# Kernel tuning notes

Measured on AMD Instinct MI355X. Metric: run time of the kernel, lower is better.

## Reference

```python
import jax, jax.numpy as jnp
import numpy as np

B, S, D, H = 4, 2048, 1024, 16
DEPTH = D // H
NEG = -1e9


def setup_inputs() -> dict:
    key = jax.random.key(0)
    ks = jax.random.split(key, 9)
    scale = 1.0 / np.sqrt(D)
    x = jax.random.normal(ks[0], (B, S, D), dtype=jnp.float32)
    # causal additive mask: 1 where future positions (masked), 0 elsewhere
    mask = jnp.triu(jnp.ones((S, S), dtype=jnp.float32), k=1)[None, None, :, :]
    wq = jax.random.normal(ks[1], (D, D), dtype=jnp.float32) * scale
    bq = jnp.zeros((D,), dtype=jnp.float32)
    wk = jax.random.normal(ks[2], (D, D), dtype=jnp.float32) * scale
    bk = jnp.zeros((D,), dtype=jnp.float32)
    wv = jax.random.normal(ks[3], (D, D), dtype=jnp.float32) * scale
    bv = jnp.zeros((D,), dtype=jnp.float32)
    wo = jax.random.normal(ks[4], (D, D), dtype=jnp.float32) * scale
    bo = jnp.zeros((D,), dtype=jnp.float32)
    return {"x": x, "mask": mask, "wq": wq, "bq": bq, "wk": wk, "bk": bk,
            "wv": wv, "bv": bv, "wo": wo, "bo": bo}


def _split_heads(t):
    # [B, S, D] -> [B, H, S, depth]
    return t.reshape(B, S, H, DEPTH).transpose(0, 2, 1, 3)


def reference(x, mask, wq, bq, wk, bk, wv, bv, wo, bo):
    q = _split_heads(x @ wq.T + bq)
    k = _split_heads(x @ wk.T + bk)
    v = _split_heads(x @ wv.T + bv)
    scores = jnp.einsum('bhqd,bhkd->bhqk', q, k) / jnp.sqrt(jnp.float32(DEPTH))
    scores = scores + mask * NEG
    attn = jax.nn.softmax(scores, axis=-1)
    out = jnp.einsum('bhqk,bhkd->bhqd', attn, v)  # [B, H, S, depth]
    out = out.transpose(0, 2, 1, 3).reshape(B, S, D)
    return out @ wo.T + bo
```

## Files before the change

### kernel.cpp

```cpp
#include <hip/hip_runtime.h>
#include <hip/hip_bf16.h>
#include <stdint.h>

typedef __attribute__((ext_vector_type(8))) short short8;
typedef __attribute__((ext_vector_type(4))) float f32x4;
typedef __attribute__((ext_vector_type(16))) float f32x16;

#define AS1 __attribute__((address_space(1)))
#define AS3 __attribute__((address_space(3)))

constexpr int Bc = 4, Sc = 2048, Dc = 1024, Hc = 16;

__device__ __forceinline__ unsigned short f2b(float x) {
  __hip_bfloat16 h = __float2bfloat16(x);
  return *reinterpret_cast<unsigned short*>(&h);
}

__device__ __forceinline__ uint32_t cvtpk(float lo, float hi) {
  uint32_t r;
  asm("v_cvt_pk_bf16_f32 %0, %1, %2" : "=v"(r) : "v"(lo), "v"(hi));
  return r;
}

__device__ __forceinline__ void glds16(const void* g, void* l) {
  __builtin_amdgcn_global_load_lds((const AS1 uint32_t*)g, (AS3 uint32_t*)l, 16, 0, 0);
}

__global__ void cast_f32_bf16_x4(const float* __restrict__ in,
                                 unsigned short* __restrict__ out, int n4) {
  int i = blockIdx.x * blockDim.x + threadIdx.x;
  if (i >= n4) return;
  float4 a = ((const float4*)in)[i];
  ushort4 o;
  o.x = f2b(a.x); o.y = f2b(a.y); o.z = f2b(a.z); o.w = f2b(a.w);
  ((ushort4*)out)[i] = o;
}

__global__ void cast_w4(const float* __restrict__ wq, const float* __restrict__ wk,
                        const float* __restrict__ wv, const float* __restrict__ wo,
                        unsigned short* __restrict__ oq, unsigned short* __restrict__ ok,
                        unsigned short* __restrict__ ov, unsigned short* __restrict__ oo) {
  int which = blockIdx.y;
  const float* in = which == 0 ? wq : which == 1 ? wk : which == 2 ? wv : wo;
  unsigned short* out = which == 0 ? oq : which == 1 ? ok : which == 2 ? ov : oo;
  int i = blockIdx.x * blockDim.x + threadIdx.x;
  float4 a = ((const float4*)in)[i];
  ushort4 o;
  o.x = f2b(a.x); o.y = f2b(a.y); o.z = f2b(a.z); o.w = f2b(a.w);
  ((ushort4*)out)[i] = o;
}

template<int MODE>
__device__ __forceinline__ void gemm128_b32(
    const unsigned short* __restrict__ A, const unsigned short* __restrict__ W,
    const float* __restrict__ bias, void* __restrict__ outp,
    int m0, int n0, unsigned short* lA, unsigned short* lB)
{
  const int tid = threadIdx.x;
  const int w = tid >> 6, lane = tid & 63;
  const int g = lane >> 4, c = lane & 15;
  const int wr = w >> 1, wc = w & 1;

  f32x4 acc[4][4];
#pragma unroll
  for (int i = 0; i < 4; ++i)
#pragma unroll
    for (int j = 0; j < 4; ++j) acc[i][j] = f32x4{0.f, 0.f, 0.f, 0.f};

  const int srow = lane >> 2;
  const int schunk = (lane & 3) * 8;

  for (int k0 = 0; k0 < 1024; k0 += 32) {
#pragma unroll
    for (int i = 0; i < 2; ++i) {
      int row = i * 64 + w * 16 + srow;
      glds16(A + (size_t)(m0 + row) * 1024 + k0 + schunk,
             (char*)lA + i * 4096 + w * 1024);
      glds16(W + (size_t)(n0 + row) * 1024 + k0 + schunk,
             (char*)lB + i * 4096 + w * 1024);
    }
    __syncthreads();

    short8 aF[4], bF[4];
#pragma unroll
    for (int mt = 0; mt < 4; ++mt) {
      int row = wr * 64 + mt * 16 + c;
      aF[mt] = *(const short8*)&lA[row * 32 + g * 8];
    }
#pragma unroll
    for (int nt = 0; nt < 4; ++nt) {
      int row = wc * 64 + nt * 16 + c;
      bF[nt] = *(const short8*)&lB[row * 32 + g * 8];
    }
#pragma unroll
    for (int mt = 0; mt < 4; ++mt)
#pragma unroll
      for (int nt = 0; nt < 4; ++nt)
        acc[mt][nt] = __builtin_amdgcn_mfma_f32_16x16x32_bf16(aF[mt], bF[nt],
                                                              acc[mt][nt], 0, 0, 0);
    __syncthreads();
  }

#pragma unroll
  for (int mt = 0; mt < 4; ++mt) {
    int mg = m0 + wr * 64 + mt * 16 + 4 * g;
#pragma unroll
    for (int nt = 0; nt < 4; ++nt) {
      int ng = n0 + wc * 64 + nt * 16 + c;
      float bb_ = bias[ng];
      if constexpr (MODE == 0) {
        unsigned short* o = (unsigned short*)outp;
#pragma unroll
        for (int r = 0; r < 4; ++r)
          o[(size_t)(mg + r) * 1024 + ng] = f2b(acc[mt][nt][r] + bb_);
      } else if constexpr (MODE == 1) {
        unsigned short* o = (unsigned short*)outp;
        int bb = mg >> 11, s0 = mg & 2047;
        int hh = ng >> 6, dd = ng & 63;
        ushort4 pk;
        pk.x = f2b(acc[mt][nt][0] + bb_);
        pk.y = f2b(acc[mt][nt][1] + bb_);
        pk.z = f2b(acc[mt][nt][2] + bb_);
        pk.w = f2b(acc[mt][nt][3] + bb_);
        *(ushort4*)&o[(((size_t)bb * Hc + hh) * 64 + dd) * Sc + s0] = pk;
      } else {
        float* o = (float*)outp;
#pragma unroll
        for (int r = 0; r < 4; ++r)
          o[(size_t)(mg + r) * 1024 + ng] = acc[mt][nt][r] + bb_;
      }
    }
  }
}

template<int MODE>
__device__ __forceinline__ void gemm128_b64(
    const unsigned short* __restrict__ A, const unsigned short* __restrict__ W,
    const float* __restrict__ bias, void* __restrict__ outp,
    int m0, int n0, unsigned short* lA, unsigned short* lB)
{
  const int tid = threadIdx.x;
  const int w = tid >> 6, lane = tid & 63;
  const int g = lane >> 4, c = lane & 15;
  const int wr = w >> 1, wc = w & 1;

  f32x4 acc[4][4];
#pragma unroll
  for (int i = 0; i < 4; ++i)
#pragma unroll
    for (int j = 0; j < 4; ++j) acc[i][j] = f32x4{0.f, 0.f, 0.f, 0.f};

  const int lrow8 = lane >> 3;
  const int gslot = (lane & 7) ^ lrow8;

  const unsigned short* ap[4];
  const unsigned short* bp[4];
#pragma unroll
  for (int j = 0; j < 4; ++j) {
    int row = (j * 4 + w) * 8 + lrow8;
    ap[j] = A + (size_t)(m0 + row) * 1024 + gslot * 8;
    bp[j] = W + (size_t)(n0 + row) * 1024 + gslot * 8;
  }

  const int sl0 = (g ^ (c & 7)) << 4;
  const int sl1 = ((4 ^ g) ^ (c & 7)) << 4;
  const char* lA0 = (const char*)lA + (wr * 64 + c) * 128 + sl0;
  const char* lA1 = (const char*)lA + (wr * 64 + c) * 128 + sl1;
  const char* lB0 = (const char*)lB + (wc * 64 + c) * 128 + sl0;
  const char* lB1 = (const char*)lB + (wc * 64 + c) * 128 + sl1;

#define STAGE64                                             \
  do {                                                      \
    _Pragma("unroll")                                       \
    for (int j = 0; j < 4; ++j) {                           \
      glds16(ap[j], (char*)lA + (j * 4 + w) * 1024);        \
      glds16(bp[j], (char*)lB + (j * 4 + w) * 1024);        \
      ap[j] += 64; bp[j] += 64;                             \
    }                                                       \
  } while (0)

  STAGE64;
  for (int t = 0; t < 16; ++t) {
    asm volatile("s_waitcnt vmcnt(0)" ::: "memory");
    __builtin_amdgcn_s_barrier();
    asm volatile("" ::: "memory");

#pragma unroll
    for (int ks = 0; ks < 2; ++ks) {
      short8 aF[4], bF[4];
#pragma unroll
      for (int mt = 0; mt < 4; ++mt)
        aF[mt] = *(const short8*)((ks ? lA1 : lA0) + mt * 2048);
#pragma unroll
      for (int nt = 0; nt < 4; ++nt)
        bF[nt] = *(const short8*)((ks ? lB1 : lB0) + nt * 2048);
#pragma unroll
      for (int mt = 0; mt < 4; ++mt)
#pragma unroll
        for (int nt = 0; nt < 4; ++nt)
          acc[mt][nt] = __builtin_amdgcn_mfma_f32_16x16x32_bf16(
              aF[mt], bF[nt], acc[mt][nt], 0, 0, 0);
    }
    asm volatile("" ::: "memory");
    __builtin_amdgcn_s_barrier();
    asm volatile("" ::: "memory");
    if (t + 1 < 16) STAGE64;
  }
#undef STAGE64

#pragma unroll
  for (int mt = 0; mt < 4; ++mt) {
    int mg = m0 + wr * 64 + mt * 16 + 4 * g;
#pragma unroll
    for (int nt = 0; nt < 4; ++nt) {
      int ng = n0 + wc * 64 + nt * 16 + c;
      float bb_ = bias[ng];
      if constexpr (MODE == 2) {
        float* o = (float*)outp;
#pragma unroll
        for (int r = 0; r < 4; ++r)
          o[(size_t)(mg + r) * 1024 + ng] = acc[mt][nt][r] + bb_;
      } else {
        unsigned short* o = (unsigned short*)outp;
#pragma unroll
        for (int r = 0; r < 4; ++r)
          o[(size_t)(mg + r) * 1024 + ng] = f2b(acc[mt][nt][r] + bb_);
      }
    }
  }
}

__global__ __launch_bounds__(256) void qkv_gemm(
    const unsigned short* __restrict__ xb,
    const unsigned short* __restrict__ wqb, const unsigned short* __restrict__ wkb,
    const unsigned short* __restrict__ wvb,
    const float* __restrict__ bq, const float* __restrict__ bk,
    const float* __restrict__ bv,
    unsigned short* __restrict__ qo, unsigned short* __restrict__ ko,
    unsigned short* __restrict__ vto)
{
  __shared__ unsigned short lA[128 * 32], lB[128 * 32];
  int m0 = blockIdx.x * 128;
  int which = blockIdx.y >> 3;
  int n0 = (blockIdx.y & 7) * 128;
  if (which == 0)      gemm128_b32<0>(xb, wqb, bq, qo, m0, n0, lA, lB);
  else if (which == 1) gemm128_b32<0>(xb, wkb, bk, ko, m0, n0, lA, lB);
  else                 gemm128_b32<1>(xb, wvb, bv, vto, m0, n0, lA, lB);
}

__global__ __launch_bounds__(256) void out_gemm(
    const unsigned short* __restrict__ ao, const unsigned short* __restrict__ wob,
    const float* __restrict__ bo, float* __restrict__ out)
{
  __shared__ unsigned short lA[128 * 64], lB[128 * 64];
  gemm128_b64<2>(ao, wob, bo, out, blockIdx.x * 128, blockIdx.y * 128, lA, lB);
}

__global__ __launch_bounds__(256, 2) void attn_kernel(
    const unsigned short* __restrict__ qg, const unsigned short* __restrict__ kg,
    const unsigned short* __restrict__ vtg, unsigned short* __restrict__ ao)
{
  __shared__ unsigned short lK[2][64 * 64];
  __shared__ unsigned short lV[2][64 * 64];

  const int bh = blockIdx.x;
  const int qlo = blockIdx.y, qhi = 15 - qlo;
  const int b = bh >> 4, h = bh & 15;
  const int tid = threadIdx.x, w = tid >> 6, lane = tid & 63;
  const int qr = lane & 31, hi = lane >> 5;
  const int qb2[2] = { qlo * 128 + 32 * w, qhi * 128 + 32 * w };
  constexpr float CE = 0.125f * 1.44269504f;

  short8 qB[2][4];
#pragma unroll
  for (int qi = 0; qi < 2; ++qi) {
    const unsigned short* qp = qg + (size_t)(b * Sc + qb2[qi] + qr) * Dc + h * 64 + 8 * hi;
#pragma unroll
    for (int i = 0; i < 4; ++i)
      qB[qi][i] = *(const short8*)(qp + 16 * i);
  }

  float m_[2] = { -3e38f, -3e38f }, lv[2] = { 0.f, 0.f };
  f32x16 oT[2][2];
#pragma unroll
  for (int qi = 0; qi < 2; ++qi)
#pragma unroll
    for (int n = 0; n < 2; ++n)
#pragma unroll
      for (int r = 0; r < 16; ++r) oT[qi][n][r] = 0.f;

  const int srow8 = lane >> 3;
  const int sslot = lane & 7;
  const unsigned short* kb_ = kg + (size_t)b * Sc * Dc + h * 64;
  const unsigned short* vb_ = vtg + (size_t)bh * 64 * Sc;

  auto stage = [&](int buf, int t) {
    const int kv0 = t * 64;
#pragma unroll
    for (int i = 0; i < 2; ++i) {
      int row = i * 32 + w * 8 + srow8;
      int gch = sslot ^ (row & 7);
      glds16(kb_ + (size_t)(kv0 + row) * Dc + gch * 8,
             (char*)lK[buf] + i * 4096 + w * 1024);
      glds16(vb_ + (size_t)row * Sc + kv0 + gch * 8,
             (char*)lV[buf] + i * 4096 + w * 1024);
    }
  };

  const int ntl = 2 * (qhi + 1);
  stage(0, 0);
  asm volatile("s_waitcnt vmcnt(0)" ::: "memory");
  __builtin_amdgcn_s_barrier();
  asm volatile("" ::: "memory");

  for (int t = 0; t < ntl; ++t) {
    const int cur = t & 1;
    const int kv0 = t * 64;
    if (t + 1 < ntl) stage(cur ^ 1, t + 1);

    if (kv0 <= qb2[1] + 31) {
      short8 kA[2][4];
#pragma unroll
      for (int kblk = 0; kblk < 2; ++kblk) {
        const int row = kblk * 32 + qr;
        const int swz = (row & 7) << 4;
#pragma unroll
        for (int i = 0; i < 4; ++i)
          kA[kblk][i] = *(const short8*)((const char*)lK[cur] + row * 128 +
                          (((2 * i + hi) * 16) ^ swz));
      }

      short8 pB[2][4];
      bool act[2];
#pragma unroll
      for (int qi = 0; qi < 2; ++qi) {
        const int qbase = qb2[qi];
        act[qi] = (kv0 <= qbase + 31);
        if (!act[qi]) continue;

        f32x16 sT[2];
        __builtin_amdgcn_s_setprio(1);
#pragma unroll
        for (int kblk = 0; kblk < 2; ++kblk) {
          f32x16 s;
#pragma unroll
          for (int r = 0; r < 16; ++r) s[r] = 0.f;
#pragma unroll
          for (int i = 0; i < 4; ++i)
            s = __builtin_amdgcn_mfma_f32_32x32x16_bf16(kA[kblk][i], qB[qi][i],
                                                        s, 0, 0, 0);
          sT[kblk] = s;
        }
        __builtin_amdgcn_s_setprio(0);

        if (kv0 + 63 > qbase) {
          const int q = qbase + qr;
#pragma unroll
          for (int kblk = 0; kblk < 2; ++kblk)
#pragma unroll
            for (int r = 0; r < 16; ++r) {
              int k = kv0 + kblk * 32 + (r & 3) + 8 * (r >> 2) + 4 * hi;
              if (k > q) sT[kblk][r] = -1e30f;
            }
        }

        float mx = sT[0][0];
#pragma unroll
        for (int r = 1; r < 16; ++r) mx = fmaxf(mx, sT[0][r]);
#pragma unroll
        for (int r = 0; r < 16; ++r) mx = fmaxf(mx, sT[1][r]);
        mx = fmaxf(mx, __shfl_xor(mx, 32));

        if (!__all(mx <= m_[qi] + 64.f)) {
          const float mo = m_[qi];
          const float mn = fmaxf(mo, mx);
          const float sf = __builtin_amdgcn_exp2f((mo - mn) * CE);
          m_[qi] = mn;
          lv[qi] *= sf;
#pragma unroll
          for (int n = 0; n < 2; ++n)
#pragma unroll
            for (int r = 0; r < 16; ++r) oT[qi][n][r] *= sf;
        }
        const float mc = m_[qi] * CE;
        float ls = 0.f;
#pragma unroll
        for (int kblk = 0; kblk < 2; ++kblk)
#pragma unroll
          for (int r = 0; r < 16; ++r) {
            float p = __builtin_amdgcn_exp2f(sT[kblk][r] * CE - mc);
            sT[kblk][r] = p;
            ls += p;
          }
        lv[qi] += ls;

#pragma unroll
        for (int kblk = 0; kblk < 2; ++kblk) {
          uint32_t pk[4][2];
#pragma unroll
          for (int qp = 0; qp < 4; ++qp)
#pragma unroll
            for (int rp = 0; rp < 2; ++rp)
              pk[qp][rp] = cvtpk(sT[kblk][4 * qp + 2 * rp],
                                 sT[kblk][4 * qp + 2 * rp + 1]);
#pragma unroll
          for (int m2 = 0; m2 < 2; ++m2) {
            uint32_t s0 = hi ? pk[2 * m2][0] : pk[2 * m2 + 1][0];
            uint32_t s1 = hi ? pk[2 * m2][1] : pk[2 * m2 + 1][1];
            uint32_t r0 = __shfl_xor(s0, 32);
            uint32_t r1 = __shfl_xor(s1, 32);
            uint32_t w0 = hi ? r0 : pk[2 * m2][0];
            uint32_t w1 = hi ? r1 : pk[2 * m2][1];
            uint32_t w2 = hi ? pk[2 * m2 + 1][0] : r0;
            uint32_t w3 = hi ? pk[2 * m2 + 1][1] : r1;
            uint32_t tmp[4] = { w0, w1, w2, w3 };
            pB[qi][2 * kblk + m2] = *(const short8*)tmp;
          }
        }
      }

      short8 vA[2][4];
#pragma unroll
      for (int n = 0; n < 2; ++n) {
        const int row = 32 * n + qr;
        const int swz = (row & 7) << 4;
#pragma unroll
        for (int m = 0; m < 4; ++m)
          vA[n][m] = *(const short8*)((const char*)lV[cur] + row * 128 +
                       (((2 * m + hi) * 16) ^ swz));
      }

      __builtin_amdgcn_s_setprio(1);
#pragma unroll
      for (int qi = 0; qi < 2; ++qi) {
        if (!act[qi]) continue;
#pragma unroll
        for (int n = 0; n < 2; ++n)
#pragma unroll
          for (int m = 0; m < 4; ++m)
            oT[qi][n] = __builtin_amdgcn_mfma_f32_32x32x16_bf16(
                vA[n][m], pB[qi][m], oT[qi][n], 0, 0, 0);
      }
      __builtin_amdgcn_s_setprio(0);
    }

    asm volatile("s_waitcnt vmcnt(0)" ::: "memory");
    __builtin_amdgcn_s_barrier();
    asm volatile("" ::: "memory");
  }

#pragma unroll
  for (int qi = 0; qi < 2; ++qi) {
    float l = lv[qi] + __shfl_xor(lv[qi], 32);
    float inv = 1.0f / l;
    const int qrow = qb2[qi] + qr;
    unsigned short* op = ao + (size_t)(b * Sc + qrow) * Dc + h * 64;
#pragma unroll
    for (int n = 0; n < 2; ++n)
#pragma unroll
      for (int rg = 0; rg < 4; ++rg) {
        ushort4 pkv;
        pkv.x = f2b(oT[qi][n][4 * rg + 0] * inv);
        pkv.y = f2b(oT[qi][n][4 * rg + 1] * inv);
        pkv.z = f2b(oT[qi][n][4 * rg + 2] * inv);
        pkv.w = f2b(oT[qi][n][4 * rg + 3] * inv);
        *(ushort4*)(op + 32 * n + 8 * rg + 4 * hi) = pkv;
      }
  }
}

extern "C" void kernel_launch(void* const* d_in, const int* in_sizes, int n_in,
                              void* d_out, int out_size, void* d_ws, size_t ws_size,
                              hipStream_t stream) {
  const float* x  = (const float*)d_in[0];
  const float* wq = (const float*)d_in[2];
  const float* bq = (const float*)d_in[3];
  const float* wk = (const float*)d_in[4];
  const float* bk = (const float*)d_in[5];
  const float* wv = (const float*)d_in[6];
  const float* bv = (const float*)d_in[7];
  const float* wo = (const float*)d_in[8];
  const float* bo = (const float*)d_in[9];
  float* out = (float*)d_out;

  char* ws = (char*)d_ws;
  unsigned short* xb  = (unsigned short*)(ws);
  unsigned short* wqb = (unsigned short*)(ws + 16777216);
  unsigned short* wkb = (unsigned short*)(ws + 18874368);
  unsigned short* wvb = (unsigned short*)(ws + 20971520);
  unsigned short* wob = (unsigned short*)(ws + 23068672);
  unsigned short* qb  = (unsigned short*)(ws + 25165824);
  unsigned short* kb  = (unsigned short*)(ws + 41943040);
  unsigned short* vtb = (unsigned short*)(ws + 58720256);
  unsigned short* aob = (unsigned short*)(ws + 75497472);

  cast_f32_bf16_x4<<<8192, 256, 0, stream>>>(x, xb, 2097152);
  cast_w4<<<dim3(1024, 4), 256, 0, stream>>>(wq, wk, wv, wo, wqb, wkb, wvb, wob);

  qkv_gemm<<<dim3(64, 24), 256, 0, stream>>>(xb, wqb, wkb, wvb, bq, bk, bv,
                                             qb, kb, vtb);
  attn_kernel<<<dim3(64, 8), 256, 0, stream>>>(qb, kb, vtb, aob);
  out_gemm<<<dim3(64, 8), 256, 0, stream>>>(aob, wob, bo, out);
}
```

Baseline: 163.6 us.

## Split paired causal query tiles into separate blocks with higher occupancy

The attention kernel previously gave each block a pair of query tiles (low and high) so that causal work was balanced across blocks. It now gives each block a single 128-row query tile, launches twice as many blocks in heaviest-first order, and raises the occupancy hint to 4 blocks per CU. This lowers register pressure and exposes more parallelism. In exchange, K/V tiles are no longer shared between the two query tiles, so K/V loads to LDS roughly double, and per-block work becomes unbalanced.

```diff
diff --git a/kernel.cpp b/kernel.cpp
--- a/kernel.cpp
+++ b/kernel.cpp
@@ -256,7 +256,7 @@
   gemm128_b64<2>(ao, wob, bo, out, blockIdx.x * 128, blockIdx.y * 128, lA, lB);
 }
 
-__global__ __launch_bounds__(256, 2) void attn_kernel(
+__global__ __launch_bounds__(256, 4) void attn_kernel(
     const unsigned short* __restrict__ qg, const unsigned short* __restrict__ kg,
     const unsigned short* __restrict__ vtg, unsigned short* __restrict__ ao)
 {
@@ -264,30 +264,27 @@
   __shared__ unsigned short lV[2][64 * 64];
 
   const int bh = blockIdx.x;
-  const int qlo = blockIdx.y, qhi = 15 - qlo;
+  const int qt = 15 - blockIdx.y;
   const int b = bh >> 4, h = bh & 15;
   const int tid = threadIdx.x, w = tid >> 6, lane = tid & 63;
   const int qr = lane & 31, hi = lane >> 5;
-  const int qb2[2] = { qlo * 128 + 32 * w, qhi * 128 + 32 * w };
+  const int qbase = qt * 128 + 32 * w;
   constexpr float CE = 0.125f * 1.44269504f;
 
-  short8 qB[2][4];
-#pragma unroll
-  for (int qi = 0; qi < 2; ++qi) {
-    const unsigned short* qp = qg + (size_t)(b * Sc + qb2[qi] + qr) * Dc + h * 64 + 8 * hi;
+  short8 qB[4];
+  {
+    const unsigned short* qp = qg + (size_t)(b * Sc + qbase + qr) * Dc + h * 64 + 8 * hi;
 #pragma unroll
     for (int i = 0; i < 4; ++i)
-      qB[qi][i] = *(const short8*)(qp + 16 * i);
-  }
-
-  float m_[2] = { -3e38f, -3e38f }, lv[2] = { 0.f, 0.f };
-  f32x16 oT[2][2];
-#pragma unroll
-  for (int qi = 0; qi < 2; ++qi)
-#pragma unroll
-    for (int n = 0; n < 2; ++n)
-#pragma unroll
-      for (int r = 0; r < 16; ++r) oT[qi][n][r] = 0.f;
+      qB[i] = *(const short8*)(qp + 16 * i);
+  }
+
+  float m_ = -3e38f, lv = 0.f;
+  f32x16 oT[2];
+#pragma unroll
+  for (int n = 0; n < 2; ++n)
+#pragma unroll
+    for (int r = 0; r < 16; ++r) oT[n][r] = 0.f;
 
   const int srow8 = lane >> 3;
   const int sslot = lane & 7;
@@ -307,7 +304,7 @@
     }
   };
 
-  const int ntl = 2 * (qhi + 1);
+  const int ntl = 2 * (qt + 1);
   stage(0, 0);
   asm volatile("s_waitcnt vmcnt(0)" ::: "memory");
   __builtin_amdgcn_s_barrier();
@@ -318,7 +315,7 @@
     const int kv0 = t * 64;
     if (t + 1 < ntl) stage(cur ^ 1, t + 1);
 
-    if (kv0 <= qb2[1] + 31) {
+    if (kv0 <= qbase + 31) {
       short8 kA[2][4];
 #pragma unroll
       for (int kblk = 0; kblk < 2; ++kblk) {
@@ -330,92 +327,84 @@
                           (((2 * i + hi) * 16) ^ swz));
       }
 
-      short8 pB[2][4];
-      bool act[2];
-#pragma unroll
-      for (int qi = 0; qi < 2; ++qi) {
-        const int qbase = qb2[qi];
-        act[qi] = (kv0 <= qbase + 31);
-        if (!act[qi]) continue;
-
-        f32x16 sT[2];
-        __builtin_amdgcn_s_setprio(1);
-#pragma unroll
-        for (int kblk = 0; kblk < 2; ++kblk) {
-          f32x16 s;
-#pragma unroll
-          for (int r = 0; r < 16; ++r) s[r] = 0.f;
-#pragma unroll
-          for (int i = 0; i < 4; ++i)
-            s = __builtin_amdgcn_mfma_f32_32x32x16_bf16(kA[kblk][i], qB[qi][i],
-                                                        s, 0, 0, 0);
-          sT[kblk] = s;
+      f32x16 sT[2];
+      __builtin_amdgcn_s_setprio(1);
+#pragma unroll
+      for (int kblk = 0; kblk < 2; ++kblk) {
+        f32x16 s;
+#pragma unroll
+        for (int r = 0; r < 16; ++r) s[r] = 0.f;
+#pragma unroll
+        for (int i = 0; i < 4; ++i)
+          s = __builtin_amdgcn_mfma_f32_32x32x16_bf16(kA[kblk][i], qB[i],
+                                                      s, 0, 0, 0);
+        sT[kblk] = s;
+      }
+      __builtin_amdgcn_s_setprio(0);
+
+      if (kv0 + 63 > qbase) {
+        const int q = qbase + qr;
+#pragma unroll
+        for (int kblk = 0; kblk < 2; ++kblk)
+#pragma unroll
+          for (int r = 0; r < 16; ++r) {
+            int k = kv0 + kblk * 32 + (r & 3) + 8 * (r >> 2) + 4 * hi;
+            if (k > q) sT[kblk][r] = -1e30f;
+          }
+      }
+
+      float mx = sT[0][0];
+#pragma unroll
+      for (int r = 1; r < 16; ++r) mx = fmaxf(mx, sT[0][r]);
+#pragma unroll
+      for (int r = 0; r < 16; ++r) mx = fmaxf(mx, sT[1][r]);
+      mx = fmaxf(mx, __shfl_xor(mx, 32));
+
+      if (!__all(mx <= m_ + 64.f)) {
+        const float mo = m_;
+        const float mn = fmaxf(mo, mx);
+        const float sf = __builtin_amdgcn_exp2f((mo - mn) * CE);
+        m_ = mn;
+        lv *= sf;
+#pragma unroll
+        for (int n = 0; n < 2; ++n)
+#pragma unroll
+          for (int r = 0; r < 16; ++r) oT[n][r] *= sf;
+      }
+      const float mc = m_ * CE;
+      float ls = 0.f;
+#pragma unroll
+      for (int kblk = 0; kblk < 2; ++kblk)
+#pragma unroll
+        for (int r = 0; r < 16; ++r) {
+          float p = __builtin_amdgcn_exp2f(sT[kblk][r] * CE - mc);
+          sT[kblk][r] = p;
+          ls += p;
         }
-        __builtin_amdgcn_s_setprio(0);
-
-        if (kv0 + 63 > qbase) {
-          const int q = qbase + qr;
-#pragma unroll
-          for (int kblk = 0; kblk < 2; ++kblk)
-#pragma unroll
-            for (int r = 0; r < 16; ++r) {
-              int k = kv0 + kblk * 32 + (r & 3) + 8 * (r >> 2) + 4 * hi;
-              if (k > q) sT[kblk][r] = -1e30f;
-            }
-        }
-
-        float mx = sT[0][0];
-#pragma unroll
-        for (int r = 1; r < 16; ++r) mx = fmaxf(mx, sT[0][r]);
-#pragma unroll
-        for (int r = 0; r < 16; ++r) mx = fmaxf(mx, sT[1][r]);
-        mx = fmaxf(mx, __shfl_xor(mx, 32));
-
-        if (!__all(mx <= m_[qi] + 64.f)) {
-          const float mo = m_[qi];
-          const float mn = fmaxf(mo, mx);
-          const float sf = __builtin_amdgcn_exp2f((mo - mn) * CE);
-          m_[qi] = mn;
-          lv[qi] *= sf;
-#pragma unroll
-          for (int n = 0; n < 2; ++n)
-#pragma unroll
-            for (int r = 0; r < 16; ++r) oT[qi][n][r] *= sf;
-        }
-        const float mc = m_[qi] * CE;
-        float ls = 0.f;
-#pragma unroll
-        for (int kblk = 0; kblk < 2; ++kblk)
-#pragma unroll
-          for (int r = 0; r < 16; ++r) {
-            float p = __builtin_amdgcn_exp2f(sT[kblk][r] * CE - mc);
-            sT[kblk][r] = p;
-            ls += p;
-          }
-        lv[qi] += ls;
-
-#pragma unroll
-        for (int kblk = 0; kblk < 2; ++kblk) {
-          uint32_t pk[4][2];
-#pragma unroll
-          for (int qp = 0; qp < 4; ++qp)
-#pragma unroll
-            for (int rp = 0; rp < 2; ++rp)
-              pk[qp][rp] = cvtpk(sT[kblk][4 * qp + 2 * rp],
-                                 sT[kblk][4 * qp + 2 * rp + 1]);
-#pragma unroll
-          for (int m2 = 0; m2 < 2; ++m2) {
-            uint32_t s0 = hi ? pk[2 * m2][0] : pk[2 * m2 + 1][0];
-            uint32_t s1 = hi ? pk[2 * m2][1] : pk[2 * m2 + 1][1];
-            uint32_t r0 = __shfl_xor(s0, 32);
-            uint32_t r1 = __shfl_xor(s1, 32);
-            uint32_t w0 = hi ? r0 : pk[2 * m2][0];
-            uint32_t w1 = hi ? r1 : pk[2 * m2][1];
-            uint32_t w2 = hi ? pk[2 * m2 + 1][0] : r0;
-            uint32_t w3 = hi ? pk[2 * m2 + 1][1] : r1;
-            uint32_t tmp[4] = { w0, w1, w2, w3 };
-            pB[qi][2 * kblk + m2] = *(const short8*)tmp;
-          }
+      lv += ls;
+
+      short8 pB[4];
+#pragma unroll
+      for (int kblk = 0; kblk < 2; ++kblk) {
+        uint32_t pk[4][2];
+#pragma unroll
+        for (int qp = 0; qp < 4; ++qp)
+#pragma unroll
+          for (int rp = 0; rp < 2; ++rp)
+            pk[qp][rp] = cvtpk(sT[kblk][4 * qp + 2 * rp],
+                               sT[kblk][4 * qp + 2 * rp + 1]);
+#pragma unroll
+        for (int m2 = 0; m2 < 2; ++m2) {
+          uint32_t s0 = hi ? pk[2 * m2][0] : pk[2 * m2 + 1][0];
+          uint32_t s1 = hi ? pk[2 * m2][1] : pk[2 * m2 + 1][1];
+          uint32_t r0 = __shfl_xor(s0, 32);
+          uint32_t r1 = __shfl_xor(s1, 32);
+          uint32_t w0 = hi ? r0 : pk[2 * m2][0];
+          uint32_t w1 = hi ? r1 : pk[2 * m2][1];
+          uint32_t w2 = hi ? pk[2 * m2 + 1][0] : r0;
+          uint32_t w3 = hi ? pk[2 * m2 + 1][1] : r1;
+          uint32_t tmp[4] = { w0, w1, w2, w3 };
+          pB[2 * kblk + m2] = *(const short8*)tmp;
         }
       }
 
@@ -432,15 +421,11 @@
 
       __builtin_amdgcn_s_setprio(1);
 #pragma unroll
-      for (int qi = 0; qi < 2; ++qi) {
-        if (!act[qi]) continue;
-#pragma unroll
-        for (int n = 0; n < 2; ++n)
-#pragma unroll
-          for (int m = 0; m < 4; ++m)
-            oT[qi][n] = __builtin_amdgcn_mfma_f32_32x32x16_bf16(
-                vA[n][m], pB[qi][m], oT[qi][n], 0, 0, 0);
-      }
+      for (int n = 0; n < 2; ++n)
+#pragma unroll
+        for (int m = 0; m < 4; ++m)
+          oT[n] = __builtin_amdgcn_mfma_f32_32x32x16_bf16(
+              vA[n][m], pB[m], oT[n], 0, 0, 0);
       __builtin_amdgcn_s_setprio(0);
     }
 
@@ -449,21 +434,20 @@
     asm volatile("" ::: "memory");
   }
 
-#pragma unroll
-  for (int qi = 0; qi < 2; ++qi) {
-    float l = lv[qi] + __shfl_xor(lv[qi], 32);
+  {
+    float l = lv + __shfl_xor(lv, 32);
     float inv = 1.0f / l;
-    const int qrow = qb2[qi] + qr;
+    const int qrow = qbase + qr;
     unsigned short* op = ao + (size_t)(b * Sc + qrow) * Dc + h * 64;
 #pragma unroll
     for (int n = 0; n < 2; ++n)
 #pragma unroll
       for (int rg = 0; rg < 4; ++rg) {
         ushort4 pkv;
-        pkv.x = f2b(oT[qi][n][4 * rg + 0] * inv);
-        pkv.y = f2b(oT[qi][n][4 * rg + 1] * inv);
-        pkv.z = f2b(oT[qi][n][4 * rg + 2] * inv);
-        pkv.w = f2b(oT[qi][n][4 * rg + 3] * inv);
+        pkv.x = f2b(oT[n][4 * rg + 0] * inv);
+        pkv.y = f2b(oT[n][4 * rg + 1] * inv);
+        pkv.z = f2b(oT[n][4 * rg + 2] * inv);
+        pkv.w = f2b(oT[n][4 * rg + 3] * inv);
         *(ushort4*)(op + 32 * n + 8 * rg + 4 * hi) = pkv;
       }
   }
@@ -499,6 +483,6 @@
 
   qkv_gemm<<<dim3(64, 24), 256, 0, stream>>>(xb, wqb, wkb, wvb, bq, bk, bv,
                                              qb, kb, vtb);
-  attn_kernel<<<dim3(64, 8), 256, 0, stream>>>(qb, kb, vtb, aob);
+  attn_kernel<<<dim3(64, 16), 256, 0, stream>>>(qb, kb, vtb, aob);
   out_gemm<<<dim3(64, 8), 256, 0, stream>>>(aob, wob, bo, out);
 }
```

New measurement: 163.2 us. No clear change (-0.3%).
